# Performance work log

Hardware: AMD Instinct MI355X
Metric: run time of the kernel (lower is better)

Reference implementation:

```python
import jax, jax.numpy as jnp
import numpy as np

BLOCKSIZE = 128
NUM_EXPERTS = 16
TOP_K = 6
HIDDEN = 2048
INTER = 1408
TOKENS = 4096
N_BLK_H = HIDDEN // BLOCKSIZE   # 16
N_BLK_I = -(-INTER // BLOCKSIZE)  # 11 (ceil)


def setup_inputs() -> dict:
    key = jax.random.key(0)
    ks = jax.random.split(key, 8)
    x = jax.random.normal(ks[0], (TOKENS, HIDDEN), dtype=jnp.float32)
    selected_experts = jax.random.randint(ks[1], (TOKENS, TOP_K), 0, NUM_EXPERTS)
    # quantized-style weights + per-block scales (dequant = w * repeat(s, blocksize))
    w0 = jax.random.normal(ks[2], (NUM_EXPERTS, INTER, HIDDEN), dtype=jnp.float32) * 0.02
    s0 = jax.random.uniform(ks[3], (NUM_EXPERTS, INTER, N_BLK_H), dtype=jnp.float32, minval=0.5, maxval=1.5)
    w1 = jax.random.normal(ks[4], (NUM_EXPERTS, INTER, HIDDEN), dtype=jnp.float32) * 0.02
    s1 = jax.random.uniform(ks[5], (NUM_EXPERTS, INTER, N_BLK_H), dtype=jnp.float32, minval=0.5, maxval=1.5)
    w2 = jax.random.normal(ks[6], (NUM_EXPERTS, HIDDEN, INTER), dtype=jnp.float32) * 0.02
    s2 = jax.random.uniform(ks[7], (NUM_EXPERTS, HIDDEN, N_BLK_I), dtype=jnp.float32, minval=0.5, maxval=1.5)
    return {"x": x, "selected_experts": selected_experts,
            "w0": w0, "s0": s0, "w1": w1, "s1": s1, "w2": w2, "s2": s2}


def _dequant(w, s):
    # w: [E, O, I], s: [E, O, ceil(I/bs)] -> broadcast each scale over its block
    s_full = jnp.repeat(s, BLOCKSIZE, axis=-1)[..., : w.shape[-1]]
    return w * s_full


def reference(x, selected_experts, w0, s0, w1, s1, w2, s2):
    # Dequantize block-quantized expert weights.
    W0 = _dequant(w0, s0)  # gate proj [E, I, H]
    W1 = _dequant(w1, s1)  # up proj   [E, I, H]
    W2 = _dequant(w2, s2)  # down proj [E, H, I]
    # Original loops token x slot, calling expert(x[i]). Equivalent batched form:
    # compute every expert on every token, then gather by (token, slot) index.
    gate = jnp.einsum('th,eih->eti', x, W0)            # [E, T, I]
    up = jnp.einsum('th,eih->eti', x, W1)              # [E, T, I]
    act = jax.nn.silu(gate) * up                       # [E, T, I]
    all_out = jnp.einsum('eti,ehi->eth', act, W2)      # [E, T, H]
    tok = jnp.arange(x.shape[0])[:, None]              # [T, 1]
    out = all_out[selected_experts, tok]               # [T, K, H]
    return out
```

## Files before the change

### kernel.cpp

```cpp
#include <hip/hip_runtime.h>
#include <stdint.h>

#define TOKENS 4096
#define HIDDEN 2048
#define INTER  1408
#define NEXP   16
#define TOPK   6
#define NPAIR  (TOKENS*TOPK)
#define BM     128
#define MAXTILES (NPAIR/BM + NEXP)
#define MAXT2  (NPAIR/256 + NEXP)
#define NT1    (INTER/128)
#define NT2    (HIDDEN/128)
#define NT2W   (HIDDEN/256)

typedef __attribute__((ext_vector_type(8))) short bf16x8;
typedef __attribute__((ext_vector_type(4))) float f32x4;

__device__ __forceinline__ short f2bf(float f){
  union { float f; uint32_t u; } v; v.f = f;
  uint32_t r = (v.u + 0x7FFFu + ((v.u >> 16) & 1u)) >> 16;
  return (short)(r & 0xFFFFu);
}

__device__ __forceinline__ void gld16(const void* g, const void* l){
  __builtin_amdgcn_global_load_lds((const __attribute__((address_space(1))) void*)g,
                                   (__attribute__((address_space(3))) void*)l, 16, 0, 0);
}

__device__ __forceinline__ f32x4 ntld4(const float* p){
  return __builtin_nontemporal_load((const f32x4*)p);
}

#define SB() __builtin_amdgcn_sched_barrier(0)
#define BAR() __builtin_amdgcn_s_barrier()
#define WAITV(n) asm volatile("s_waitcnt vmcnt(" #n ")" ::: "memory")
#define WAITL() asm volatile("s_waitcnt lgkmcnt(0)" ::: "memory")


__global__ void k_xcast(const float* __restrict__ x, short* __restrict__ xb){
  int i = (blockIdx.x * 256 + threadIdx.x) * 8;
  f32x4 a = ntld4(x + i);
  f32x4 b = ntld4(x + i + 4);
  bf16x8 o;
  #pragma unroll
  for (int j = 0; j < 4; ++j){ o[j] = f2bf(a[j]); o[4+j] = f2bf(b[j]); }
  *(bf16x8*)(xb + i) = o;
}

__global__ void k_deq01(const float* __restrict__ w0, const float* __restrict__ s0,
                        const float* __restrict__ w1, const float* __restrict__ s1,
                        short* __restrict__ o0, short* __restrict__ o1){
  int row = blockIdx.x;
  const float* w; const float* s; short* o;
  if (row < NEXP * INTER){ w = w0; s = s0; o = o0; }
  else { row -= NEXP * INTER; w = w1; s = s1; o = o1; }
  const size_t base = (size_t)row * HIDDEN;
  const int c = threadIdx.x * 8;
  float sc = s[(size_t)row * (HIDDEN/128) + (c >> 7)];
  f32x4 a = ntld4(w + base + c);
  f32x4 b = ntld4(w + base + c + 4);
  bf16x8 h;
  #pragma unroll
  for (int j = 0; j < 4; ++j){ h[j] = f2bf(a[j] * sc); h[4+j] = f2bf(b[j] * sc); }
  *(bf16x8*)(o + base + c) = h;
}

__global__ void k_deqw2(const float* __restrict__ w2, const float* __restrict__ s2,
                        short* __restrict__ o){
  const int total = NEXP * HIDDEN * (INTER / 8);
  for (int gi = blockIdx.x * 256 + threadIdx.x; gi < total; gi += gridDim.x * 256){
    int row = gi / (INTER / 8);
    int c = (gi - row * (INTER / 8)) * 8;
    const size_t base = (size_t)row * INTER;
    float sc = s2[(size_t)row * 11 + (c >> 7)];
    f32x4 a = ntld4(w2 + base + c);
    f32x4 b = ntld4(w2 + base + c + 4);
    bf16x8 h;
    #pragma unroll
    for (int j = 0; j < 4; ++j){ h[j] = f2bf(a[j] * sc); h[4+j] = f2bf(b[j] * sc); }
    *(bf16x8*)(o + base + c) = h;
  }
}

__global__ void k_dequant(const float* __restrict__ w, const float* __restrict__ s,
                          short* __restrict__ o, int rowlen, int nblk){
  const int row = blockIdx.x;
  const size_t base = (size_t)row * rowlen;
  for (int c = threadIdx.x * 8; c < rowlen; c += blockDim.x * 8){
    float sc = s[(size_t)row * nblk + (c >> 7)];
    f32x4 a = *(const f32x4*)(w + base + c);
    f32x4 b = *(const f32x4*)(w + base + c + 4);
    bf16x8 h;
    #pragma unroll
    for (int j = 0; j < 4; ++j){ h[j] = f2bf(a[j] * sc); h[4+j] = f2bf(b[j] * sc); }
    *(bf16x8*)(o + base + c) = h;
  }
}

__global__ void k_count(const int* __restrict__ sel, int* __restrict__ cnt){
  int p = blockIdx.x * 256 + threadIdx.x;
  if (p < NPAIR) atomicAdd(&cnt[sel[p]], 1);
}

__global__ void k_scan(const int* __restrict__ cnt, int* __restrict__ offsets,
                       int2* __restrict__ tiles, int* __restrict__ ntiles,
                       int2* __restrict__ tiles2, int* __restrict__ ntiles2){
  if (threadIdx.x != 0) return;
  int off = 0, nt = 0, nt2 = 0;
  for (int e = 0; e < NEXP; ++e){
    offsets[e] = off;
    int c = cnt[e];
    for (int m = 0; m < c; m += BM){
      int rows = c - m; if (rows > BM) rows = BM;
      tiles[nt++] = make_int2(off + m, (e << 16) | rows);
    }
    for (int m = 0; m < c; m += 256){
      int rows = c - m; if (rows > 256) rows = 256;
      tiles2[nt2++] = make_int2(off + m, (e << 16) | rows);
    }
    off += c;
  }
  offsets[NEXP] = off;
  *ntiles = nt;
  *ntiles2 = nt2;
}

__global__ void k_scatter(const int* __restrict__ sel, const int* __restrict__ offsets,
                          int* __restrict__ cursor, int* __restrict__ pair_tk){
  int p = blockIdx.x * 256 + threadIdx.x;
  if (p >= NPAIR) return;
  int e = sel[p];
  int pos = offsets[e] + atomicAdd(&cursor[e], 1);
  pair_tk[pos] = (p / TOPK) * 8 + (p % TOPK);
}


__global__ __launch_bounds__(512) void k_g1(
    const short* __restrict__ xb,
    const short* __restrict__ w0b, const short* __restrict__ w1b,
    const int2* __restrict__ tiles2, const int* __restrict__ ntiles2,
    const int* __restrict__ pair_tk, short* __restrict__ act)
{
  const int nwg = MAXT2 * NT1;
  const int orig = (int)(blockIdx.y * MAXT2 + blockIdx.x);
  const int wg = (orig & 7) * (nwg >> 3) + (orig >> 3);
  const int tx = wg % MAXT2, ty = wg / MAXT2;
  if (tx >= *ntiles2) return;
  const int2 td = tiles2[tx];
  const int mstart = td.x;
  const int e  = td.y >> 16;
  const int vr = td.y & 0xFFFF;

  __shared__ short lA[4][8192];
  __shared__ short lB[4][8192];

  const int tid = threadIdx.x, w = tid >> 6, lane = tid & 63;

  const short* pA[2]; const short* pB[2]; int sg8[2];
  #pragma unroll
  for (int i = 0; i < 2; ++i){
    int s = (w * 2 + i) * 64 + lane;
    int r = s >> 2, j = (s & 3) ^ ((s >> 3) & 3);
    sg8[i] = s * 8;
    int p = mstart + r; if (p >= NPAIR) p = NPAIR - 1;
    pA[i] = xb + (size_t)(pair_tk[p] >> 3) * HIDDEN + j * 8;
    int G = r >> 4, srow = (G >> 1) * 16 + (r & 15);
    const short* wsrc = (G & 1) ? w1b : w0b;
    pB[i] = wsrc + ((size_t)e * INTER + (size_t)ty * 128 + srow) * HIDDEN + j * 8;
  }
  auto stage = [&](int slot, int ko){
    #pragma unroll
    for (int i = 0; i < 2; ++i) gld16(pA[i] + ko, &lA[slot][sg8[i]]);
    #pragma unroll
    for (int i = 0; i < 2; ++i) gld16(pB[i] + ko, &lB[slot][sg8[i]]);
  };

  f32x4 acc[4][8];
  #pragma unroll
  for (int i = 0; i < 4; ++i)
    #pragma unroll
    for (int j = 0; j < 8; ++j) acc[i][j] = (f32x4)0.f;

  const int cc = lane & 15, ks = lane >> 4;
  const int sx = (ks ^ ((cc >> 1) & 3)) * 8;
  const int wm = w >> 1, wn = w & 1;
  int arow[4], brow[8];
  #pragma unroll
  for (int mf = 0; mf < 4; ++mf) arow[mf] = (wm * 64 + mf * 16 + cc) * 32;
  #pragma unroll
  for (int nf = 0; nf < 8; ++nf) brow[nf] = (wn * 128 + nf * 16 + cc) * 32;

  stage(0, 0); stage(1, 32); stage(2, 64); stage(3, 96);

  #pragma unroll 1
  for (int t = 0; t < 32; ++t){
    const int b = t & 1;
    if (t == 0)      { WAITV(12); }
    else if (t < 31) { WAITV(8);  }
    else             { WAITV(4);  }
    SB(); BAR(); SB();
    {
      bf16x8 a0[4], bb[8];
      #pragma unroll
      for (int mf = 0; mf < 4; ++mf) a0[mf] = *(const bf16x8*)&lA[b*2][arow[mf] + sx];
      #pragma unroll
      for (int nf = 0; nf < 8; ++nf) bb[nf] = *(const bf16x8*)&lB[b*2][brow[nf] + sx];
      if (t >= 1 && t + 1 < 32) stage(((t+1)&1)*2 + 1, (t+1)*64 + 32);
      WAITL(); SB();
      __builtin_amdgcn_s_setprio(1);
      #pragma unroll
      for (int nf = 0; nf < 8; ++nf)
        #pragma unroll
        for (int mf = 0; mf < 4; ++mf)
          acc[mf][nf] = __builtin_amdgcn_mfma_f32_16x16x32_bf16(a0[mf], bb[nf], acc[mf][nf], 0, 0, 0);
      __builtin_amdgcn_s_setprio(0);
      SB(); BAR(); SB();
    }
    if (t < 31) { WAITV(8); } else { WAITV(0); }
    SB(); BAR(); SB();
    {
      bf16x8 a0[4], bb[8];
      #pragma unroll
      for (int mf = 0; mf < 4; ++mf) a0[mf] = *(const bf16x8*)&lA[b*2+1][arow[mf] + sx];
      #pragma unroll
      for (int nf = 0; nf < 8; ++nf) bb[nf] = *(const bf16x8*)&lB[b*2+1][brow[nf] + sx];
      if (t + 2 < 32) stage(b*2, (t+2)*64);
      WAITL(); SB();
      __builtin_amdgcn_s_setprio(1);
      #pragma unroll
      for (int nf = 0; nf < 8; ++nf)
        #pragma unroll
        for (int mf = 0; mf < 4; ++mf)
          acc[mf][nf] = __builtin_amdgcn_mfma_f32_16x16x32_bf16(a0[mf], bb[nf], acc[mf][nf], 0, 0, 0);
      __builtin_amdgcn_s_setprio(0);
      SB(); BAR(); SB();
    }
  }

  #pragma unroll
  for (int mf = 0; mf < 4; ++mf){
    #pragma unroll
    for (int j = 0; j < 4; ++j){
      int row = wm * 64 + mf * 16 + ks * 4 + j;
      if (row < vr){
        short* ar = act + (size_t)(mstart + row) * INTER + (size_t)ty * 128 + cc;
        #pragma unroll
        for (int q = 0; q < 4; ++q){
          float g = acc[mf][2*q][j], u = acc[mf][2*q+1][j];
          float a = g / (1.f + __expf(-g)) * u;
          __builtin_nontemporal_store(f2bf(a), &ar[(wn * 4 + q) * 16]);
        }
      }
    }
  }
}

__global__ __launch_bounds__(512) void k_g2(
    const short* __restrict__ act, const short* __restrict__ w2b,
    const int2* __restrict__ tiles2, const int* __restrict__ ntiles2,
    const int* __restrict__ pair_tk, float* __restrict__ out)
{
  const int nwg = MAXT2 * NT2W;
  const int orig = (int)(blockIdx.y * MAXT2 + blockIdx.x);
  const int wg = (orig & 7) * (nwg >> 3) + (orig >> 3);
  const int tx = wg % MAXT2, ty = wg / MAXT2;
  if (tx >= *ntiles2) return;
  const int2 td = tiles2[tx];
  const int mstart = td.x;
  const int e  = td.y >> 16;
  const int vr = td.y & 0xFFFF;

  __shared__ short lA[4][8192];
  __shared__ short lB[4][8192];

  const int tid = threadIdx.x, w = tid >> 6, lane = tid & 63;

  const short* pA[2]; const short* pB[2]; int sg8[2];
  #pragma unroll
  for (int i = 0; i < 2; ++i){
    int s = (w * 2 + i) * 64 + lane;
    int r = s >> 2, j = (s & 3) ^ ((s >> 3) & 3);
    sg8[i] = s * 8;
    int p = mstart + r; if (p >= NPAIR) p = NPAIR - 1;
    pA[i] = act + (size_t)p * INTER + j * 8;
    pB[i] = w2b + ((size_t)e * HIDDEN + (size_t)ty * 256 + r) * INTER + j * 8;
  }
  auto stage = [&](int slot, int ko){
    #pragma unroll
    for (int i = 0; i < 2; ++i) gld16(pA[i] + ko, &lA[slot][sg8[i]]);
    #pragma unroll
    for (int i = 0; i < 2; ++i) gld16(pB[i] + ko, &lB[slot][sg8[i]]);
  };

  f32x4 acc[4][8];
  #pragma unroll
  for (int i = 0; i < 4; ++i)
    #pragma unroll
    for (int j = 0; j < 8; ++j) acc[i][j] = (f32x4)0.f;

  const int cc = lane & 15, ks = lane >> 4;
  const int sx = (ks ^ ((cc >> 1) & 3)) * 8;
  const int wm = w >> 1, wn = w & 1;
  int arow[4], brow[8];
  #pragma unroll
  for (int mf = 0; mf < 4; ++mf) arow[mf] = (wm * 64 + mf * 16 + cc) * 32;
  #pragma unroll
  for (int nf = 0; nf < 8; ++nf) brow[nf] = (wn * 128 + nf * 16 + cc) * 32;

  stage(0, 0); stage(1, 32); stage(2, 64); stage(3, 96);

  #pragma unroll 1
  for (int t = 0; t < 22; ++t){
    const int b = t & 1;
    if (t == 0)      { WAITV(12); }
    else if (t < 21) { WAITV(8);  }
    else             { WAITV(4);  }
    SB(); BAR(); SB();
    {
      bf16x8 a0[4], bb[8];
      #pragma unroll
      for (int mf = 0; mf < 4; ++mf) a0[mf] = *(const bf16x8*)&lA[b*2][arow[mf] + sx];
      #pragma unroll
      for (int nf = 0; nf < 8; ++nf) bb[nf] = *(const bf16x8*)&lB[b*2][brow[nf] + sx];
      if (t >= 1 && t + 1 < 22) stage(((t+1)&1)*2 + 1, (t+1)*64 + 32);
      WAITL(); SB();
      __builtin_amdgcn_s_setprio(1);
      #pragma unroll
      for (int nf = 0; nf < 8; ++nf)
        #pragma unroll
        for (int mf = 0; mf < 4; ++mf)
          acc[mf][nf] = __builtin_amdgcn_mfma_f32_16x16x32_bf16(a0[mf], bb[nf], acc[mf][nf], 0, 0, 0);
      __builtin_amdgcn_s_setprio(0);
      SB(); BAR(); SB();
    }
    if (t < 21) { WAITV(8); } else { WAITV(0); }
    SB(); BAR(); SB();
    {
      bf16x8 a0[4], bb[8];
      #pragma unroll
      for (int mf = 0; mf < 4; ++mf) a0[mf] = *(const bf16x8*)&lA[b*2+1][arow[mf] + sx];
      #pragma unroll
      for (int nf = 0; nf < 8; ++nf) bb[nf] = *(const bf16x8*)&lB[b*2+1][brow[nf] + sx];
      if (t + 2 < 22) stage(b*2, (t+2)*64);
      WAITL(); SB();
      __builtin_amdgcn_s_setprio(1);
      #pragma unroll
      for (int nf = 0; nf < 8; ++nf)
        #pragma unroll
        for (int mf = 0; mf < 4; ++mf)
          acc[mf][nf] = __builtin_amdgcn_mfma_f32_16x16x32_bf16(a0[mf], bb[nf], acc[mf][nf], 0, 0, 0);
      __builtin_amdgcn_s_setprio(0);
      SB(); BAR(); SB();
    }
  }

  #pragma unroll
  for (int mf = 0; mf < 4; ++mf){
    #pragma unroll
    for (int j = 0; j < 4; ++j){
      int row = wm * 64 + mf * 16 + ks * 4 + j;
      if (row < vr){
        int ptk = pair_tk[mstart + row];
        float* orow = out + ((size_t)(ptk >> 3) * TOPK + (ptk & 7)) * HIDDEN
                      + (size_t)ty * 256 + wn * 128 + cc;
        #pragma unroll
        for (int nf = 0; nf < 8; ++nf)
          __builtin_nontemporal_store(acc[mf][nf][j], &orow[nf * 16]);
      }
    }
  }
}


__global__ __launch_bounds__(256) void k_gemm1(
    const short* __restrict__ xb,
    const float* __restrict__ w0, const float* __restrict__ s0,
    const float* __restrict__ w1, const float* __restrict__ s1,
    const int2* __restrict__ tiles, const int* __restrict__ ntiles,
    const int* __restrict__ pair_tk, short* __restrict__ act)
{
  if ((int)blockIdx.x >= *ntiles) return;
  const int2 td = tiles[blockIdx.x];
  const int mstart = td.x;
  const int e  = td.y >> 16;
  const int vr = td.y & 0xFFFF;
  const int tid = threadIdx.x;
  const int lane = tid & 63;

  __shared__ short lA[BM * 32];
  __shared__ short lB0[BM * 40];
  __shared__ short lB1[BM * 40];

  const int r0 = tid >> 2, r1 = 64 + (tid >> 2);
  const int seg = tid & 3;
  int p0 = mstart + r0; if (p0 >= NPAIR) p0 = NPAIR - 1;
  int p1 = mstart + r1; if (p1 >= NPAIR) p1 = NPAIR - 1;
  const short* arow0 = xb + (size_t)(pair_tk[p0] >> 3) * HIDDEN + (seg ^ ((r0 >> 1) & 3)) * 8;
  const short* arow1 = xb + (size_t)(pair_tk[p1] >> 3) * HIDDEN + (seg ^ ((r1 >> 1) & 3)) * 8;
  const short* ldsA0 = &lA[tid * 8];
  const short* ldsA1 = &lA[2048 + tid * 8];

  const int brow = tid >> 1, half = tid & 1;
  const int gbrow = blockIdx.y * BM + brow;
  const float* w0row = w0 + ((size_t)e * INTER + gbrow) * HIDDEN + half * 16;
  const float* w1row = w1 + ((size_t)e * INTER + gbrow) * HIDDEN + half * 16;
  const float* s0row = s0 + ((size_t)e * INTER + gbrow) * (HIDDEN / 128);
  const float* s1row = s1 + ((size_t)e * INTER + gbrow) * (HIDDEN / 128);
  short* lb0w = &lB0[brow * 40 + half * 16];
  short* lb1w = &lB1[brow * 40 + half * 16];

  f32x4 acc0[4][4], acc1[4][4];
  #pragma unroll
  for (int i = 0; i < 4; ++i)
    #pragma unroll
    for (int j = 0; j < 4; ++j){ acc0[i][j] = (f32x4)0.f; acc1[i][j] = (f32x4)0.f; }

  const int wm = tid >> 7, wn = (tid >> 6) & 1;
  const int cc = lane & 15, ks = lane >> 4;

  for (int kt = 0; kt < HIDDEN / 32; ++kt){
    gld16(arow0 + kt * 32, ldsA0);
    gld16(arow1 + kt * 32, ldsA1);
    {
      float sc = s0row[kt >> 2];
      const float* g = w0row + kt * 32;
      f32x4 q0 = *(const f32x4*)g,       q1 = *(const f32x4*)(g + 4),
            q2 = *(const f32x4*)(g + 8), q3 = *(const f32x4*)(g + 12);
      bf16x8 h0, h1;
      #pragma unroll
      for (int i = 0; i < 4; ++i){
        h0[i] = f2bf(q0[i] * sc); h0[4 + i] = f2bf(q1[i] * sc);
        h1[i] = f2bf(q2[i] * sc); h1[4 + i] = f2bf(q3[i] * sc);
      }
      *(bf16x8*)lb0w = h0; *(bf16x8*)(lb0w + 8) = h1;
    }
    {
      float sc = s1row[kt >> 2];
      const float* g = w1row + kt * 32;
      f32x4 q0 = *(const f32x4*)g,       q1 = *(const f32x4*)(g + 4),
            q2 = *(const f32x4*)(g + 8), q3 = *(const f32x4*)(g + 12);
      bf16x8 h0, h1;
      #pragma unroll
      for (int i = 0; i < 4; ++i){
        h0[i] = f2bf(q0[i] * sc); h0[4 + i] = f2bf(q1[i] * sc);
        h1[i] = f2bf(q2[i] * sc); h1[4 + i] = f2bf(q3[i] * sc);
      }
      *(bf16x8*)lb1w = h0; *(bf16x8*)(lb1w + 8) = h1;
    }
    __syncthreads();

    bf16x8 af[4];
    #pragma unroll
    for (int mf = 0; mf < 4; ++mf){
      int row = wm * 64 + mf * 16 + cc;
      af[mf] = *(const bf16x8*)&lA[row * 32 + ((ks ^ ((row >> 1) & 3)) * 8)];
    }
    #pragma unroll
    for (int nf = 0; nf < 4; ++nf){
      int rb = wn * 64 + nf * 16 + cc;
      bf16x8 b0 = *(const bf16x8*)&lB0[rb * 40 + ks * 8];
      bf16x8 b1 = *(const bf16x8*)&lB1[rb * 40 + ks * 8];
      #pragma unroll
      for (int mf = 0; mf < 4; ++mf)
        acc0[mf][nf] = __builtin_amdgcn_mfma_f32_16x16x32_bf16(af[mf], b0, acc0[mf][nf], 0, 0, 0);
      #pragma unroll
      for (int mf = 0; mf < 4; ++mf)
        acc1[mf][nf] = __builtin_amdgcn_mfma_f32_16x16x32_bf16(af[mf], b1, acc1[mf][nf], 0, 0, 0);
    }
    __syncthreads();
  }

  const int rbase = wm * 64 + (lane >> 4) * 4;
  #pragma unroll
  for (int mf = 0; mf < 4; ++mf){
    #pragma unroll
    for (int j = 0; j < 4; ++j){
      int row = rbase + mf * 16 + j;
      if (row < vr){
        short* ar = act + (size_t)(mstart + row) * INTER + blockIdx.y * BM + wn * 64 + cc;
        #pragma unroll
        for (int nf = 0; nf < 4; ++nf){
          float g = acc0[mf][nf][j], u = acc1[mf][nf][j];
          float a = g / (1.f + __expf(-g)) * u;
          ar[nf * 16] = f2bf(a);
        }
      }
    }
  }
}

__global__ __launch_bounds__(256) void k_gemm2(
    const short* __restrict__ act,
    const float* __restrict__ w2, const float* __restrict__ s2,
    const int2* __restrict__ tiles, const int* __restrict__ ntiles,
    const int* __restrict__ pair_tk, float* __restrict__ out)
{
  if ((int)blockIdx.x >= *ntiles) return;
  const int2 td = tiles[blockIdx.x];
  const int mstart = td.x;
  const int e  = td.y >> 16;
  const int vr = td.y & 0xFFFF;
  const int tid = threadIdx.x;
  const int lane = tid & 63;

  __shared__ short lA[BM * 32];
  __shared__ short lB[BM * 40];

  const int r0 = tid >> 2, r1 = 64 + (tid >> 2);
  const int seg = tid & 3;
  int p0 = mstart + r0; if (p0 >= NPAIR) p0 = NPAIR - 1;
  int p1 = mstart + r1; if (p1 >= NPAIR) p1 = NPAIR - 1;
  const short* arow0 = act + (size_t)p0 * INTER + (seg ^ ((r0 >> 1) & 3)) * 8;
  const short* arow1 = act + (size_t)p1 * INTER + (seg ^ ((r1 >> 1) & 3)) * 8;
  const short* ldsA0 = &lA[tid * 8];
  const short* ldsA1 = &lA[2048 + tid * 8];

  const int brow = tid >> 1, half = tid & 1;
  const int gbrow = blockIdx.y * BM + brow;
  const float* w2row = w2 + ((size_t)e * HIDDEN + gbrow) * INTER + half * 16;
  const float* s2row = s2 + ((size_t)e * HIDDEN + gbrow) * 11;
  short* lbw = &lB[brow * 40 + half * 16];

  f32x4 acc[4][4];
  #pragma unroll
  for (int i = 0; i < 4; ++i)
    #pragma unroll
    for (int j = 0; j < 4; ++j) acc[i][j] = (f32x4)0.f;

  const int wm = tid >> 7, wn = (tid >> 6) & 1;
  const int cc = lane & 15, ks = lane >> 4;

  for (int kt = 0; kt < INTER / 32; ++kt){
    gld16(arow0 + kt * 32, ldsA0);
    gld16(arow1 + kt * 32, ldsA1);
    {
      float sc = s2row[kt >> 2];
      const float* g = w2row + kt * 32;
      f32x4 q0 = *(const f32x4*)g,       q1 = *(const f32x4*)(g + 4),
            q2 = *(const f32x4*)(g + 8), q3 = *(const f32x4*)(g + 12);
      bf16x8 h0, h1;
      #pragma unroll
      for (int i = 0; i < 4; ++i){
        h0[i] = f2bf(q0[i] * sc); h0[4 + i] = f2bf(q1[i] * sc);
        h1[i] = f2bf(q2[i] * sc); h1[4 + i] = f2bf(q3[i] * sc);
      }
      *(bf16x8*)lbw = h0; *(bf16x8*)(lbw + 8) = h1;
    }
    __syncthreads();

    bf16x8 af[4];
    #pragma unroll
    for (int mf = 0; mf < 4; ++mf){
      int row = wm * 64 + mf * 16 + cc;
      af[mf] = *(const bf16x8*)&lA[row * 32 + ((ks ^ ((row >> 1) & 3)) * 8)];
    }
    #pragma unroll
    for (int nf = 0; nf < 4; ++nf){
      int rb = wn * 64 + nf * 16 + cc;
      bf16x8 b = *(const bf16x8*)&lB[rb * 40 + ks * 8];
      #pragma unroll
      for (int mf = 0; mf < 4; ++mf)
        acc[mf][nf] = __builtin_amdgcn_mfma_f32_16x16x32_bf16(af[mf], b, acc[mf][nf], 0, 0, 0);
    }
    __syncthreads();
  }

  const int rbase = wm * 64 + (lane >> 4) * 4;
  #pragma unroll
  for (int mf = 0; mf < 4; ++mf){
    #pragma unroll
    for (int j = 0; j < 4; ++j){
      int row = rbase + mf * 16 + j;
      if (row < vr){
        int ptk = pair_tk[mstart + row];
        float* orow = out + ((size_t)(ptk >> 3) * TOPK + (ptk & 7)) * HIDDEN
                      + blockIdx.y * BM + wn * 64 + cc;
        #pragma unroll
        for (int nf = 0; nf < 4; ++nf)
          orow[nf * 16] = acc[mf][nf][j];
      }
    }
  }
}


extern "C" void kernel_launch(void* const* d_in, const int* in_sizes, int n_in,
                              void* d_out, int out_size, void* d_ws, size_t ws_size,
                              hipStream_t stream)
{
  const float* x  = (const float*)d_in[0];
  const int*   sel= (const int*)  d_in[1];
  const float* w0 = (const float*)d_in[2];
  const float* s0 = (const float*)d_in[3];
  const float* w1 = (const float*)d_in[4];
  const float* s1 = (const float*)d_in[5];
  const float* w2 = (const float*)d_in[6];
  const float* s2 = (const float*)d_in[7];
  float* out = (float*)d_out;

  char* ws = (char*)d_ws;
  size_t o = 0;
  auto alloc = [&](size_t n){ size_t r = o; o = (o + n + 255) & ~(size_t)255; return r; };
  int*  cnt     = (int*) (ws + alloc(64));
  int*  cursor  = (int*) (ws + alloc(64));
  int*  offsets = (int*) (ws + alloc(68));
  int*  ntiles  = (int*) (ws + alloc(4));
  int*  ntiles2 = (int*) (ws + alloc(4));
  int2* tiles   = (int2*)(ws + alloc(MAXTILES * 8));
  int2* tiles2  = (int2*)(ws + alloc(MAXT2 * 8));
  int*  pair_tk = (int*) (ws + alloc((size_t)NPAIR * 4));
  short* xb     = (short*)(ws + alloc((size_t)TOKENS * HIDDEN * 2));
  short* act    = (short*)(ws + alloc((size_t)NPAIR * INTER * 2));
  const size_t WSZ = (size_t)NEXP * INTER * HIDDEN * 2;
  short* w0b    = (short*)(ws + alloc(WSZ));
  short* w1b    = (short*)(ws + alloc(WSZ));
  short* w2b    = (short*)(ws + alloc(WSZ));
  const bool predeq = (ws_size >= o);
  (void)in_sizes; (void)n_in; (void)out_size;

  hipMemsetAsync(ws, 0, 512, stream);

  k_xcast  <<<(TOKENS * HIDDEN) / (256 * 8), 256, 0, stream>>>(x, xb);
  k_count  <<<(NPAIR + 255) / 256, 256, 0, stream>>>(sel, cnt);
  k_scan   <<<1, 64, 0, stream>>>(cnt, offsets, tiles, ntiles, tiles2, ntiles2);
  k_scatter<<<(NPAIR + 255) / 256, 256, 0, stream>>>(sel, offsets, cursor, pair_tk);

  if (predeq){
    k_deq01<<<2 * NEXP * INTER, 256, 0, stream>>>(w0, s0, w1, s1, w0b, w1b);
    k_g1<<<dim3(MAXT2, NT1), 512, 0, stream>>>(xb, w0b, w1b,
                                               tiles2, ntiles2, pair_tk, act);
    k_deqw2<<<2048, 256, 0, stream>>>(w2, s2, w2b);
    k_g2<<<dim3(MAXT2, NT2W), 512, 0, stream>>>(act, w2b,
                                                tiles2, ntiles2, pair_tk, out);
  } else {
    k_gemm1<<<dim3(MAXTILES, NT1), 256, 0, stream>>>(xb, w0, s0, w1, s1,
                                                     tiles, ntiles, pair_tk, act);
    k_gemm2<<<dim3(MAXTILES, NT2), 256, 0, stream>>>(act, w2, s2,
                                                     tiles, ntiles, pair_tk, out);
  }
}
```

Measured before the change: 816.5 us.

## Restructure GEMM main loops to single barrier per half-step with shallower prefetch

Both grouped GEMM loops drop from a 4-stage prologue with two barriers per half-step to a 2-stage prologue, one barrier per half-step, and a staging slot refilled immediately after its LDS fragments are read into registers. The goal is to remove one workgroup barrier per half-step and simplify vmcnt accounting. In exchange, global prefetch depth falls from about three half-steps ahead to one, so memory latency is less hidden. Correctness depends on the single barrier also covering the write-after-read hazard on the slot being restaged.

```diff
diff --git a/kernel.cpp b/kernel.cpp
--- a/kernel.cpp
+++ b/kernel.cpp
@@ -191,22 +191,22 @@
   #pragma unroll
   for (int nf = 0; nf < 8; ++nf) brow[nf] = (wn * 128 + nf * 16 + cc) * 32;
 
-  stage(0, 0); stage(1, 32); stage(2, 64); stage(3, 96);
+  stage(0, 0); stage(1, 32);
 
   #pragma unroll 1
   for (int t = 0; t < 32; ++t){
-    const int b = t & 1;
-    if (t == 0)      { WAITV(12); }
-    else if (t < 31) { WAITV(8);  }
-    else             { WAITV(4);  }
-    SB(); BAR(); SB();
-    {
+    #pragma unroll
+    for (int h = 0; h < 2; ++h){
+      if (t == 31 && h == 1) { WAITV(0); } else { WAITV(4); }
+      SB(); BAR(); SB();
+      const short* A = lA[(t & 1) * 2 + h];
+      const short* B = lB[(t & 1) * 2 + h];
       bf16x8 a0[4], bb[8];
       #pragma unroll
-      for (int mf = 0; mf < 4; ++mf) a0[mf] = *(const bf16x8*)&lA[b*2][arow[mf] + sx];
-      #pragma unroll
-      for (int nf = 0; nf < 8; ++nf) bb[nf] = *(const bf16x8*)&lB[b*2][brow[nf] + sx];
-      if (t >= 1 && t + 1 < 32) stage(((t+1)&1)*2 + 1, (t+1)*64 + 32);
+      for (int mf = 0; mf < 4; ++mf) a0[mf] = *(const bf16x8*)&A[arow[mf] + sx];
+      #pragma unroll
+      for (int nf = 0; nf < 8; ++nf) bb[nf] = *(const bf16x8*)&B[brow[nf] + sx];
+      if (t + 1 < 32) stage(((t + 1) & 1) * 2 + h, (t + 1) * 64 + h * 32);
       WAITL(); SB();
       __builtin_amdgcn_s_setprio(1);
       #pragma unroll
@@ -215,26 +215,7 @@
         for (int mf = 0; mf < 4; ++mf)
           acc[mf][nf] = __builtin_amdgcn_mfma_f32_16x16x32_bf16(a0[mf], bb[nf], acc[mf][nf], 0, 0, 0);
       __builtin_amdgcn_s_setprio(0);
-      SB(); BAR(); SB();
-    }
-    if (t < 31) { WAITV(8); } else { WAITV(0); }
-    SB(); BAR(); SB();
-    {
-      bf16x8 a0[4], bb[8];
-      #pragma unroll
-      for (int mf = 0; mf < 4; ++mf) a0[mf] = *(const bf16x8*)&lA[b*2+1][arow[mf] + sx];
-      #pragma unroll
-      for (int nf = 0; nf < 8; ++nf) bb[nf] = *(const bf16x8*)&lB[b*2+1][brow[nf] + sx];
-      if (t + 2 < 32) stage(b*2, (t+2)*64);
-      WAITL(); SB();
-      __builtin_amdgcn_s_setprio(1);
-      #pragma unroll
-      for (int nf = 0; nf < 8; ++nf)
-        #pragma unroll
-        for (int mf = 0; mf < 4; ++mf)
-          acc[mf][nf] = __builtin_amdgcn_mfma_f32_16x16x32_bf16(a0[mf], bb[nf], acc[mf][nf], 0, 0, 0);
-      __builtin_amdgcn_s_setprio(0);
-      SB(); BAR(); SB();
+      SB();
     }
   }
 
@@ -308,22 +289,22 @@
   #pragma unroll
   for (int nf = 0; nf < 8; ++nf) brow[nf] = (wn * 128 + nf * 16 + cc) * 32;
 
-  stage(0, 0); stage(1, 32); stage(2, 64); stage(3, 96);
+  stage(0, 0); stage(1, 32);
 
   #pragma unroll 1
   for (int t = 0; t < 22; ++t){
-    const int b = t & 1;
-    if (t == 0)      { WAITV(12); }
-    else if (t < 21) { WAITV(8);  }
-    else             { WAITV(4);  }
-    SB(); BAR(); SB();
-    {
+    #pragma unroll
+    for (int h = 0; h < 2; ++h){
+      if (t == 21 && h == 1) { WAITV(0); } else { WAITV(4); }
+      SB(); BAR(); SB();
+      const short* A = lA[(t & 1) * 2 + h];
+      const short* B = lB[(t & 1) * 2 + h];
       bf16x8 a0[4], bb[8];
       #pragma unroll
-      for (int mf = 0; mf < 4; ++mf) a0[mf] = *(const bf16x8*)&lA[b*2][arow[mf] + sx];
-      #pragma unroll
-      for (int nf = 0; nf < 8; ++nf) bb[nf] = *(const bf16x8*)&lB[b*2][brow[nf] + sx];
-      if (t >= 1 && t + 1 < 22) stage(((t+1)&1)*2 + 1, (t+1)*64 + 32);
+      for (int mf = 0; mf < 4; ++mf) a0[mf] = *(const bf16x8*)&A[arow[mf] + sx];
+      #pragma unroll
+      for (int nf = 0; nf < 8; ++nf) bb[nf] = *(const bf16x8*)&B[brow[nf] + sx];
+      if (t + 1 < 22) stage(((t + 1) & 1) * 2 + h, (t + 1) * 64 + h * 32);
       WAITL(); SB();
       __builtin_amdgcn_s_setprio(1);
       #pragma unroll
@@ -332,26 +313,7 @@
         for (int mf = 0; mf < 4; ++mf)
           acc[mf][nf] = __builtin_amdgcn_mfma_f32_16x16x32_bf16(a0[mf], bb[nf], acc[mf][nf], 0, 0, 0);
       __builtin_amdgcn_s_setprio(0);
-      SB(); BAR(); SB();
-    }
-    if (t < 21) { WAITV(8); } else { WAITV(0); }
-    SB(); BAR(); SB();
-    {
-      bf16x8 a0[4], bb[8];
-      #pragma unroll
-      for (int mf = 0; mf < 4; ++mf) a0[mf] = *(const bf16x8*)&lA[b*2+1][arow[mf] + sx];
-      #pragma unroll
-      for (int nf = 0; nf < 8; ++nf) bb[nf] = *(const bf16x8*)&lB[b*2+1][brow[nf] + sx];
-      if (t + 2 < 22) stage(b*2, (t+2)*64);
-      WAITL(); SB();
-      __builtin_amdgcn_s_setprio(1);
-      #pragma unroll
-      for (int nf = 0; nf < 8; ++nf)
-        #pragma unroll
-        for (int mf = 0; mf < 4; ++mf)
-          acc[mf][nf] = __builtin_amdgcn_mfma_f32_16x16x32_bf16(a0[mf], bb[nf], acc[mf][nf], 0, 0, 0);
-      __builtin_amdgcn_s_setprio(0);
-      SB(); BAR(); SB();
+      SB();
     }
   }
 
```

Result: no change. 808.9 us, median of 2 (-0.9%).
